# Kernel tuning notes

Measured on AMD Instinct MI355X. Metric: run time of the kernel, lower is better.

## Reference

```python
import jax, jax.numpy as jnp
import numpy as np

B, CIN, W = 4, 3, 28          # batch, in_channels, image size (= max_pos_embedding)
MID, HEADS, G, COUT = 16, 8, 4, 64
HALF = MID // 2               # row / col embedding dims


def _embed(u, w1, b1, gamma, beta, w2, b2):
    """Positional-embedding MLP applied elementwise to scalars u (N,).
    Conv2d(1->16,k=1) -> LayerNorm(16 channels) -> Swish -> Conv2d(16->MID/2,k=1)."""
    h = u[:, None] * w1[None, :] + b1                     # (N, 16)
    mu = h.mean(-1, keepdims=True)
    var = ((h - mu) ** 2).mean(-1, keepdims=True)
    h = gamma * (h - mu) / jnp.sqrt(var + 1e-5) + beta    # LayerNorm over channels
    h = h * jax.nn.sigmoid(h)                             # Swish
    return h @ w2.T + b2                                  # (N, HALF)


def _rot_indices():
    """Acted relative-position lookup indices for the 4 rotations.
    Values index into u = concat(rel, -rel) where rel = linspace(-1,1,2W-1)."""
    n = 2 * W - 1
    ar = np.arange(W)
    rel = ar[None, :] - ar[:, None] + (W - 1)             # rel[i,k] in [0, 2W-2]
    R = np.broadcast_to(rel[:, None, :, None], (W,) * 4)  # depends on (i,k)
    C = np.broadcast_to(rel[None, :, None, :], (W,) * 4)  # depends on (j,l)
    # rotation by 0/90/180/270 deg acting on (row, col) relative coordinates
    ridx = np.stack([R, C + n, R + n, C], 0)              # row component index
    cidx = np.stack([C, R, C + n, R + n], 0)              # col component index
    return jnp.asarray(ridx, jnp.int32), jnp.asarray(cidx, jnp.int32)


def setup_inputs() -> dict:
    key = jax.random.key(0)
    ks = jax.random.split(key, 24)
    def nrm(k, shape, fan):
        return jax.random.normal(k, shape, jnp.float32) / np.float32(np.sqrt(fan))
    inp = {"x": jax.random.normal(ks[0], (B, CIN, W, W), jnp.float32)}
    inp["wq"] = nrm(ks[1], (MID * HEADS, CIN), CIN); inp["bq"] = jnp.zeros((MID * HEADS,), jnp.float32)
    inp["wk"] = nrm(ks[2], (MID * HEADS, CIN), CIN); inp["bk"] = jnp.zeros((MID * HEADS,), jnp.float32)
    inp["wv"] = nrm(ks[3], (MID * HEADS, CIN), CIN); inp["bv"] = jnp.zeros((MID * HEADS,), jnp.float32)
    inp["w_out"] = nrm(ks[4], (COUT, MID * HEADS), MID * HEADS); inp["b_out"] = jnp.zeros((COUT,), jnp.float32)
    for pfx, base in (("row", 5), ("col", 12)):
        inp[f"{pfx}_w1"] = nrm(ks[base], (16,), 1)
        inp[f"{pfx}_b1"] = jnp.zeros((16,), jnp.float32)
        inp[f"{pfx}_gamma"] = jnp.ones((16,), jnp.float32)
        inp[f"{pfx}_beta"] = jnp.zeros((16,), jnp.float32)
        inp[f"{pfx}_w2"] = nrm(ks[base + 1], (HALF, 16), 16)
        inp[f"{pfx}_b2"] = jnp.zeros((HALF,), jnp.float32)
    inp["ridx"], inp["cidx"] = _rot_indices()
    return inp


def reference(x, wq, bq, wk, bk, wv, bv, w_out, b_out,
              row_w1, row_b1, row_gamma, row_beta, row_w2, row_b2,
              col_w1, col_b1, col_gamma, col_beta, col_w2, col_b2,
              ridx, cidx):
    b, c, H, Wd = x.shape
    # 1x1-conv q/k/v, viewed as (b, mid, heads, H, W)
    q = (jnp.einsum('oc,bcij->boij', wq, x) + bq[:, None, None]).reshape(b, MID, HEADS, H, Wd)
    k_ = (jnp.einsum('oc,bcij->boij', wk, x) + bk[:, None, None]).reshape(b, MID, HEADS, H, Wd)
    v = (jnp.einsum('oc,bcij->boij', wv, x) + bv[:, None, None]).reshape(b, MID, HEADS, H, Wd)

    content = jnp.einsum('bmhij,bmhkl->bhijkl', q, k_)     # (b,h,i,j,k,l)

    lin = jnp.linspace(-1.0, 1.0, 2 * Wd - 1)
    u = jnp.concatenate([lin, -lin])                       # unique relative coords
    E_row = _embed(u, row_w1, row_b1, row_gamma, row_beta, row_w2, row_b2)
    E_col = _embed(u, col_w1, col_b1, col_gamma, col_beta, col_w2, col_b2)
    row_emb = E_row[ridx]                                  # (G,i,j,k,l,HALF)
    col_emb = E_col[cidx]

    scores = jnp.einsum('bmhij,gijklm->bhgijkl', q[:, :HALF], row_emb)
    scores = scores + jnp.einsum('bmhij,gijklm->bhgijkl', q[:, HALF:], col_emb)
    scores = (scores + content[:, :, None]) / np.float32(np.sqrt(c))

    sh = scores.shape                                      # softmax over flattened (k,l)
    probs = jax.nn.softmax(scores.reshape(sh[:-2] + (-1,)), axis=-1).reshape(sh)

    out_v = jnp.einsum('bhgijkl,bmhkl->bmhgij', probs, v)  # (b,mid,heads,G,i,j)
    out_v = out_v.reshape(b, MID * HEADS, G, H, Wd)
    out = jnp.einsum('om,bmgij->bogij', w_out, out_v) + b_out[:, None, None, None]
    return out
```

## Files before the change

### kernel.cpp

```cpp
#include <hip/hip_runtime.h>
#include <hip/hip_fp16.h>

#define NPOS 784
#define WDIM 28

typedef _Float16 f16x8 __attribute__((ext_vector_type(8)));
typedef _Float16 f16x4 __attribute__((ext_vector_type(4)));
typedef float    f32x4 __attribute__((ext_vector_type(4)));

__global__ __launch_bounds__(256) void prep_kernel(
    const float* __restrict__ x,
    const float* __restrict__ wk, const float* __restrict__ bk,
    const float* __restrict__ wv, const float* __restrict__ bv,
    const float* __restrict__ w_out,
    const float* __restrict__ rw1, const float* __restrict__ rb1,
    const float* __restrict__ rga, const float* __restrict__ rbe,
    const float* __restrict__ rw2, const float* __restrict__ rb2,
    const float* __restrict__ cw1, const float* __restrict__ cb1,
    const float* __restrict__ cga, const float* __restrict__ cbe,
    const float* __restrict__ cw2, const float* __restrict__ cb2,
    _Float16* __restrict__ Kfrag, _Float16* __restrict__ Vfrag,
    _Float16* __restrict__ Wfrag,
    float* __restrict__ Etr, float* __restrict__ Etc)
{
    const int t = threadIdx.x;
    if (blockIdx.x == 416) {
        int d = -1;
        const float *w1 = rw1, *b1 = rb1, *ga = rga, *be = rbe, *w2 = rw2, *b2 = rb2;
        float* E = Etr;
        if (t < 110) { d = t; }
        else if (t >= 128 && t < 238) { d = t - 128; w1 = cw1; b1 = cb1; ga = cga; be = cbe; w2 = cw2; b2 = cb2; E = Etc; }
        if (d < 0) return;
        float u = (d < 55) ? (-1.0f + (float)d * (2.0f / 54.0f))
                           : -(-1.0f + (float)(d - 55) * (2.0f / 54.0f));
        float hb[16], mu = 0.0f;
#pragma unroll
        for (int c = 0; c < 16; ++c) { hb[c] = u * w1[c] + b1[c]; mu += hb[c]; }
        mu *= (1.0f / 16.0f);
        float var = 0.0f;
#pragma unroll
        for (int c = 0; c < 16; ++c) { float dv = hb[c] - mu; var += dv * dv; }
        var *= (1.0f / 16.0f);
        float rstd = rsqrtf(var + 1e-5f);
#pragma unroll
        for (int c = 0; c < 16; ++c) {
            float hn = ga[c] * (hb[c] - mu) * rstd + be[c];
            hb[c] = hn / (1.0f + __expf(-hn));
        }
#pragma unroll
        for (int m = 0; m < 8; ++m) {
            float e = b2[m];
#pragma unroll
            for (int c = 0; c < 16; ++c) e += hb[c] * w2[m * 16 + c];
            E[m * 110 + d] = e;
        }
        return;
    }
    if (blockIdx.x == 417) {
        for (int idx = t; idx < 8192; idx += 256) {
            int obc = idx >> 9, lane = (idx >> 3) & 63, j = idx & 7;
            int o  = (obc >> 2) * 16 + (lane & 15);
            int mh = (obc & 3) * 32 + (lane >> 4) * 8 + j;
            Wfrag[idx] = (_Float16)w_out[o * 128 + mh];
        }
        return;
    }

    const int bid  = blockIdx.x;
    const int b    = bid / 104, rem = bid - b * 104;
    const int tile = rem >> 3, h = rem & 7;
    const int lane = t & 63, mg = t >> 6;
    const int bh   = b * 8 + h;

    {
        if (t < 128) {
            int sub = (t >> 5) & 3, l32 = 32 + (t & 31);
            int qz = tile * 4 + sub;
            if (qz < 49)
                *(f16x8*)(Kfrag + ((size_t)(bh * 49 + qz) * 64 + l32) * 8) = (f16x8){};
        }
        if (tile == 12 && t < 32)
            *(f16x8*)(Vfrag + ((size_t)(bh * 25 + 24) * 64 + 32 + t) * 8) = (f16x8){};
    }

    const int ij = tile * 64 + lane;
    if (ij >= NPOS) return;

    float x0 = x[(b * 3 + 0) * NPOS + ij];
    float x1 = x[(b * 3 + 1) * NPOS + ij];
    float x2 = x[(b * 3 + 2) * NPOS + ij];

    float4 kv;
    float vv[4];
#pragma unroll
    for (int j = 0; j < 4; ++j) {
        int m = mg * 4 + j, oc = m * 8 + h;
        float w0, w1, w2v;
        w0 = wk[oc*3+0]; w1 = wk[oc*3+1]; w2v = wk[oc*3+2];
        ((float*)&kv)[j] = bk[oc] + w0*x0 + w1*x1 + w2v*x2;
        w0 = wv[oc*3+0]; w1 = wv[oc*3+1]; w2v = wv[oc*3+2];
        vv[j] = bv[oc] + w0*x0 + w1*x1 + w2v*x2;
    }
    {
        int qt = ij >> 4;
        int lp = ((mg >> 1) << 4) | (ij & 15);
        int jb = (mg & 1) * 4;
        f16x4 k4 = {(_Float16)kv.x, (_Float16)kv.y, (_Float16)kv.z, (_Float16)kv.w};
        *(f16x4*)(Kfrag + ((size_t)(bh * 49 + qt) * 64 + lp) * 8 + jb) = k4;
    }
    {
        int s5 = ij >> 5, kk = ij & 31;
        _Float16* vb = Vfrag + (((size_t)(bh * 25 + s5) * 64 + ((kk >> 3) << 4)) << 3) + (kk & 7);
#pragma unroll
        for (int j = 0; j < 4; ++j) vb[(mg * 4 + j) * 8] = (_Float16)vv[j];
    }
}

__global__ __launch_bounds__(512, 1) void attn_kernel(
    const _Float16* __restrict__ Kfrag, const _Float16* __restrict__ Vfrag,
    const _Float16* __restrict__ Wfrag,
    const float* __restrict__ Etr, const float* __restrict__ Etc,
    const float* __restrict__ x,
    const float* __restrict__ wq, const float* __restrict__ bq,
    const float* __restrict__ b_out, float* __restrict__ out)
{
    __shared__ __align__(16) unsigned char smem[56320 + 41472];
    const int t = threadIdx.x, wave = t >> 6, lane = t & 63;
    const int q15 = lane & 15, rg = lane >> 4;

    int bid = blockIdx.x;
    int xcd = bid & 7;
    int lb  = ((xcd < 4) ? xcd * 25 : 100 + (xcd - 4) * 24) + (bid >> 3);
    const int b = lb / 49, qt = lb - b * 49;
    const int bh = b * 8 + wave;
    const int q_ij = qt * 16 + q15;
    const int iq = q_ij / WDIM, jq = q_ij % WDIM;
    const float scale = 0.57735026918962576f;

    float* ebuf = (float*)(smem + 56320);
    for (int i = t; i < 1760; i += 512) ebuf[i] = (i < 880) ? Etr[i] : Etc[i - 880];

    float ql[8], qh[8];
    {
        float x0 = x[(b * 3 + 0) * NPOS + q_ij];
        float x1 = x[(b * 3 + 1) * NPOS + q_ij];
        float x2 = x[(b * 3 + 2) * NPOS + q_ij];
#pragma unroll
        for (int m = 0; m < 8; ++m) {
            int oc = m * 8 + wave;
            ql[m] = bq[oc] + wq[oc*3+0]*x0 + wq[oc*3+1]*x1 + wq[oc*3+2]*x2;
        }
#pragma unroll
        for (int m = 0; m < 8; ++m) {
            int oc = (m + 8) * 8 + wave;
            qh[m] = bq[oc] + wq[oc*3+0]*x0 + wq[oc*3+1]*x1 + wq[oc*3+2]*x2;
        }
    }
    f16x8 qf = {};
    if (rg == 0) {
#pragma unroll
        for (int j = 0; j < 8; ++j) qf[j] = (_Float16)ql[j];
    } else if (rg == 1) {
#pragma unroll
        for (int j = 0; j < 8; ++j) qf[j] = (_Float16)qh[j];
    }
    __syncthreads();

    {
        float mr = -3.0e38f, mc = -3.0e38f, m5r = -3.0e38f, m5c = -3.0e38f;
        for (int tv = 0; tv < 14; ++tv) {
            int dd = rg * 14 + tv;
            if (dd < 55) {
                float ar = 0, ac = 0, ar5 = 0, ac5 = 0;
#pragma unroll
                for (int mm = 0; mm < 8; ++mm) {
                    ar  += ql[mm] * ebuf[mm * 110 + dd];
                    ar5 += ql[mm] * ebuf[mm * 110 + dd + 55];
                    ac  += qh[mm] * ebuf[880 + mm * 110 + dd];
                    ac5 += qh[mm] * ebuf[880 + mm * 110 + dd + 55];
                }
                mr  = fmaxf(mr, ar);  mc  = fmaxf(mc, ac);
                m5r = fmaxf(m5r, ar5); m5c = fmaxf(m5c, ac5);
            }
        }
        mr  = fmaxf(mr,  __shfl_xor(mr, 16, 64));  mr  = fmaxf(mr,  __shfl_xor(mr, 32, 64));
        mc  = fmaxf(mc,  __shfl_xor(mc, 16, 64));  mc  = fmaxf(mc,  __shfl_xor(mc, 32, 64));
        m5r = fmaxf(m5r, __shfl_xor(m5r, 16, 64)); m5r = fmaxf(m5r, __shfl_xor(m5r, 32, 64));
        m5c = fmaxf(m5c, __shfl_xor(m5c, 16, 64)); m5c = fmaxf(m5c, __shfl_xor(m5c, 32, 64));
        uint2* tabw = (uint2*)smem + (wave * 16 + q15) * 55;
        for (int tv = 0; tv < 14; ++tv) {
            int dd = rg * 14 + tv;
            if (dd < 55) {
                float ar = 0, ac = 0, ar5 = 0, ac5 = 0;
#pragma unroll
                for (int mm = 0; mm < 8; ++mm) {
                    ar  += ql[mm] * ebuf[mm * 110 + dd];
                    ar5 += ql[mm] * ebuf[mm * 110 + dd + 55];
                    ac  += qh[mm] * ebuf[880 + mm * 110 + dd];
                    ac5 += qh[mm] * ebuf[880 + mm * 110 + dd + 55];
                }
                __half2 h01 = __floats2half2_rn(__expf(scale * (ar - mr)),
                                                __expf(scale * (ac - mc)));
                __half2 h23 = __floats2half2_rn(__expf(scale * (ar5 - m5r)),
                                                __expf(scale * (ac5 - m5c)));
                uint2 w; w.x = *(unsigned int*)&h01; w.y = *(unsigned int*)&h23;
                tabw[dd] = w;
            }
        }
    }
    __syncthreads();

    const f16x8* kchunk = (const f16x8*)(Kfrag + (size_t)bh * 49 * 64 * 8);

    float mx = -3.0e38f;
#pragma unroll 7
    for (int ch = 0; ch < 49; ++ch) {
        f16x8 kf = kchunk[ch * 64 + lane];
        f32x4 s = __builtin_amdgcn_mfma_f32_16x16x32_f16(kf, qf, (f32x4){0,0,0,0}, 0, 0, 0);
        mx = fmaxf(mx, fmaxf(fmaxf(s[0], s[1]), fmaxf(s[2], s[3])));
    }
    mx = fmaxf(mx, __shfl_xor(mx, 16, 64));
    mx = fmaxf(mx, __shfl_xor(mx, 32, 64));

    float ps0 = 0, ps1 = 0, ps2 = 0, ps3 = 0;
    f32x4 d0 = {0,0,0,0}, d1 = {0,0,0,0}, d2 = {0,0,0,0}, d3 = {0,0,0,0};
    _Float16* ptw = (_Float16*)(smem + 56320) + (size_t)wave * 2592;
    const uint2* tab = (const uint2*)smem + (wave * 16 + q15) * 55;
    const int prow  = (q15 & 3) * 4;
    const int tbase = (q15 >> 2) * 648;
    const f16x8* vbase = (const f16x8*)(Vfrag + (size_t)bh * 25 * 64 * 8);

    f16x8 kfA = kchunk[0 * 64 + lane];
    f16x8 kfB = kchunk[1 * 64 + lane];
    f16x8 bf  = vbase[lane];
    for (int pv = 0; pv < 25; ++pv) {
        int nA = (pv * 2 + 2 < 49) ? pv * 2 + 2 : 48;
        int nB = (pv * 2 + 3 < 49) ? pv * 2 + 3 : 48;
        int nV = (pv + 1 < 25) ? pv + 1 : 24;
        f16x8 kfA2 = kchunk[nA * 64 + lane];
        f16x8 kfB2 = kchunk[nB * 64 + lane];
        f16x8 bf2  = vbase[nV * 64 + lane];
#pragma unroll
        for (int c2 = 0; c2 < 2; ++c2) {
            int ch = pv * 2 + c2;
            float pg[4][4];
            if (ch < 49) {
                f16x8 kf = c2 ? kfB : kfA;
                f32x4 s = __builtin_amdgcn_mfma_f32_16x16x32_f16(kf, qf, (f32x4){0,0,0,0}, 0, 0, 0);
#pragma unroll
                for (int reg = 0; reg < 4; ++reg) {
                    float ec = __expf((s[reg] - mx) * scale) * 64.0f;
                    int k = ch * 16 + rg * 4 + reg;
                    int rk = (k * 2341) >> 16;
                    int ck = k - rk * WDIM;
                    uint2 tr = tab[rk - iq + 27];
                    uint2 tc = tab[ck - jq + 27];
                    float2 r01 = __half22float2(*(__half2*)&tr.x);
                    float2 r23 = __half22float2(*(__half2*)&tr.y);
                    float2 c01 = __half22float2(*(__half2*)&tc.x);
                    float2 c23 = __half22float2(*(__half2*)&tc.y);
                    pg[0][reg] = ec * r01.x * c01.y;
                    pg[1][reg] = ec * r01.y * c23.x;
                    pg[2][reg] = ec * r23.x * c23.y;
                    pg[3][reg] = ec * r23.y * c01.x;
                    ps0 += pg[0][reg]; ps1 += pg[1][reg];
                    ps2 += pg[2][reg]; ps3 += pg[3][reg];
                }
            } else {
#pragma unroll
                for (int g = 0; g < 4; ++g)
#pragma unroll
                    for (int reg = 0; reg < 4; ++reg) pg[g][reg] = 0.0f;
            }
            int cb = rg * 4 + c2 * 16;
#pragma unroll
            for (int g = 0; g < 4; ++g) {
                __half2 a01 = __floats2half2_rn(pg[g][0], pg[g][1]);
                __half2 a23 = __floats2half2_rn(pg[g][2], pg[g][3]);
                uint2 w; w.x = *(unsigned int*)&a01; w.y = *(unsigned int*)&a23;
                *(uint2*)(ptw + tbase + (prow + g) * 40 + cb) = w;
            }
        }
        f16x8 aA = *(const f16x8*)(ptw + 0 * 648 + q15 * 40 + rg * 8);
        d0 = __builtin_amdgcn_mfma_f32_16x16x32_f16(aA, bf, d0, 0, 0, 0);
        f16x8 aB = *(const f16x8*)(ptw + 1 * 648 + q15 * 40 + rg * 8);
        d1 = __builtin_amdgcn_mfma_f32_16x16x32_f16(aB, bf, d1, 0, 0, 0);
        f16x8 aC = *(const f16x8*)(ptw + 2 * 648 + q15 * 40 + rg * 8);
        d2 = __builtin_amdgcn_mfma_f32_16x16x32_f16(aC, bf, d2, 0, 0, 0);
        f16x8 aD = *(const f16x8*)(ptw + 3 * 648 + q15 * 40 + rg * 8);
        d3 = __builtin_amdgcn_mfma_f32_16x16x32_f16(aD, bf, d3, 0, 0, 0);
        kfA = kfA2; kfB = kfB2; bf = bf2;
    }
    ps0 += __shfl_xor(ps0, 16, 64); ps0 += __shfl_xor(ps0, 32, 64);
    ps1 += __shfl_xor(ps1, 16, 64); ps1 += __shfl_xor(ps1, 32, 64);
    ps2 += __shfl_xor(ps2, 16, 64); ps2 += __shfl_xor(ps2, 32, 64);
    ps3 += __shfl_xor(ps3, 16, 64); ps3 += __shfl_xor(ps3, 32, 64);
    float i0 = 1.0f / ps0, i1 = 1.0f / ps1, i2 = 1.0f / ps2, i3 = 1.0f / ps3;

    __syncthreads();
    _Float16* ovh = (_Float16*)(smem + 56320);
    {
        int mo = q15 * 8 + wave;
        int sq;
        sq = rg;
        ovh[(0*16 + sq)*136 + mo] = (_Float16)(d0[0] * __shfl(i0, sq, 64));
        ovh[(1*16 + sq)*136 + mo] = (_Float16)(d0[1] * __shfl(i1, sq, 64));
        ovh[(2*16 + sq)*136 + mo] = (_Float16)(d0[2] * __shfl(i2, sq, 64));
        ovh[(3*16 + sq)*136 + mo] = (_Float16)(d0[3] * __shfl(i3, sq, 64));
        sq = 4 + rg;
        ovh[(0*16 + sq)*136 + mo] = (_Float16)(d1[0] * __shfl(i0, sq, 64));
        ovh[(1*16 + sq)*136 + mo] = (_Float16)(d1[1] * __shfl(i1, sq, 64));
        ovh[(2*16 + sq)*136 + mo] = (_Float16)(d1[2] * __shfl(i2, sq, 64));
        ovh[(3*16 + sq)*136 + mo] = (_Float16)(d1[3] * __shfl(i3, sq, 64));
        sq = 8 + rg;
        ovh[(0*16 + sq)*136 + mo] = (_Float16)(d2[0] * __shfl(i0, sq, 64));
        ovh[(1*16 + sq)*136 + mo] = (_Float16)(d2[1] * __shfl(i1, sq, 64));
        ovh[(2*16 + sq)*136 + mo] = (_Float16)(d2[2] * __shfl(i2, sq, 64));
        ovh[(3*16 + sq)*136 + mo] = (_Float16)(d2[3] * __shfl(i3, sq, 64));
        sq = 12 + rg;
        ovh[(0*16 + sq)*136 + mo] = (_Float16)(d3[0] * __shfl(i0, sq, 64));
        ovh[(1*16 + sq)*136 + mo] = (_Float16)(d3[1] * __shfl(i1, sq, 64));
        ovh[(2*16 + sq)*136 + mo] = (_Float16)(d3[2] * __shfl(i3 == i3 ? i2 : i2, sq, 64) * 0.0f + d3[2] * __shfl(i2, sq, 64));
        ovh[(3*16 + sq)*136 + mo] = (_Float16)(d3[3] * __shfl(i3, sq, 64));
    }
    __syncthreads();

#pragma unroll
    for (int tt2 = 0; tt2 < 2; ++tt2) {
        int tl = wave * 2 + tt2;
        int ob = tl >> 2, g = tl & 3;
        f32x4 dd = {0,0,0,0};
#pragma unroll
        for (int c = 0; c < 4; ++c) {
            f16x8 wa = *(const f16x8*)(Wfrag + ((size_t)((ob * 4 + c) * 64 + lane)) * 8);
            f16x8 vb = *(const f16x8*)(ovh + (g * 16 + q15) * 136 + c * 32 + rg * 8);
            dd = __builtin_amdgcn_mfma_f32_16x16x32_f16(wa, vb, dd, 0, 0, 0);
        }
#pragma unroll
        for (int reg = 0; reg < 4; ++reg) {
            int o = ob * 16 + rg * 4 + reg;
            out[((size_t)(b * 64 + o) * 4 + g) * NPOS + qt * 16 + q15] = dd[reg] + b_out[o];
        }
    }
}

extern "C" void kernel_launch(void* const* d_in, const int* in_sizes, int n_in,
                              void* d_out, int out_size, void* d_ws, size_t ws_size,
                              hipStream_t stream)
{
    const float* x     = (const float*)d_in[0];
    const float* wq    = (const float*)d_in[1];
    const float* bq    = (const float*)d_in[2];
    const float* wk    = (const float*)d_in[3];
    const float* bk    = (const float*)d_in[4];
    const float* wv    = (const float*)d_in[5];
    const float* bv    = (const float*)d_in[6];
    const float* w_out = (const float*)d_in[7];
    const float* b_out = (const float*)d_in[8];
    const float* rw1 = (const float*)d_in[9];
    const float* rb1 = (const float*)d_in[10];
    const float* rga = (const float*)d_in[11];
    const float* rbe = (const float*)d_in[12];
    const float* rw2 = (const float*)d_in[13];
    const float* rb2 = (const float*)d_in[14];
    const float* cw1 = (const float*)d_in[15];
    const float* cb1 = (const float*)d_in[16];
    const float* cga = (const float*)d_in[17];
    const float* cbe = (const float*)d_in[18];
    const float* cw2 = (const float*)d_in[19];
    const float* cb2 = (const float*)d_in[20];

    float* Etr       = (float*)d_ws;
    float* Etc       = Etr + 880;
    _Float16* Kfrag  = (_Float16*)(Etc + 880);
    _Float16* Vfrag  = Kfrag + 802816;
    _Float16* Wfrag  = Vfrag + 409600;

    prep_kernel<<<418, 256, 0, stream>>>(x, wk, bk, wv, bv, w_out,
                                         rw1, rb1, rga, rbe, rw2, rb2,
                                         cw1, cb1, cga, cbe, cw2, cb2,
                                         Kfrag, Vfrag, Wfrag, Etr, Etc);
    attn_kernel<<<196, 512, 0, stream>>>(Kfrag, Vfrag, Wfrag, Etr, Etc,
                                         x, wq, bq, b_out, (float*)d_out);
}
```

Measured before the change: 158.8 us.

## Split key range across two wave groups per head with LDS reduction

```diff
diff --git a/kernel.cpp b/kernel.cpp
--- a/kernel.cpp
+++ b/kernel.cpp
@@ -116,7 +116,10 @@
     }
 }
 
-__global__ __launch_bounds__(512, 1) void attn_kernel(
+#define UNI_OFF 56320
+#define MX_OFF  97280
+#define PS_OFF  98304
+__global__ __launch_bounds__(1024, 1) void attn_kernel(
     const _Float16* __restrict__ Kfrag, const _Float16* __restrict__ Vfrag,
     const _Float16* __restrict__ Wfrag,
     const float* __restrict__ Etr, const float* __restrict__ Etc,
@@ -124,21 +127,22 @@
     const float* __restrict__ wq, const float* __restrict__ bq,
     const float* __restrict__ b_out, float* __restrict__ out)
 {
-    __shared__ __align__(16) unsigned char smem[56320 + 41472];
+    __shared__ __align__(16) unsigned char smem[100352];
     const int t = threadIdx.x, wave = t >> 6, lane = t & 63;
     const int q15 = lane & 15, rg = lane >> 4;
+    const int h = wave & 7, hf = wave >> 3;
 
     int bid = blockIdx.x;
     int xcd = bid & 7;
     int lb  = ((xcd < 4) ? xcd * 25 : 100 + (xcd - 4) * 24) + (bid >> 3);
     const int b = lb / 49, qt = lb - b * 49;
-    const int bh = b * 8 + wave;
+    const int bh = b * 8 + h;
     const int q_ij = qt * 16 + q15;
     const int iq = q_ij / WDIM, jq = q_ij % WDIM;
     const float scale = 0.57735026918962576f;
 
-    float* ebuf = (float*)(smem + 56320);
-    for (int i = t; i < 1760; i += 512) ebuf[i] = (i < 880) ? Etr[i] : Etc[i - 880];
+    float* ebuf = (float*)(smem + UNI_OFF);
+    for (int i = t; i < 1760; i += 1024) ebuf[i] = (i < 880) ? Etr[i] : Etc[i - 880];
 
     float ql[8], qh[8];
     {
@@ -147,12 +151,12 @@
         float x2 = x[(b * 3 + 2) * NPOS + q_ij];
 #pragma unroll
         for (int m = 0; m < 8; ++m) {
-            int oc = m * 8 + wave;
+            int oc = m * 8 + h;
             ql[m] = bq[oc] + wq[oc*3+0]*x0 + wq[oc*3+1]*x1 + wq[oc*3+2]*x2;
         }
 #pragma unroll
         for (int m = 0; m < 8; ++m) {
-            int oc = (m + 8) * 8 + wave;
+            int oc = (m + 8) * 8 + h;
             qh[m] = bq[oc] + wq[oc*3+0]*x0 + wq[oc*3+1]*x1 + wq[oc*3+2]*x2;
         }
     }
@@ -167,44 +171,35 @@
     __syncthreads();
 
     {
-        float mr = -3.0e38f, mc = -3.0e38f, m5r = -3.0e38f, m5c = -3.0e38f;
+        unsigned int* tab32 = (unsigned int*)smem + (h * 16 + q15) * 110;
+        const int d5 = hf * 55;
+        float m1 = -3.0e38f, m2 = -3.0e38f;
         for (int tv = 0; tv < 14; ++tv) {
             int dd = rg * 14 + tv;
             if (dd < 55) {
-                float ar = 0, ac = 0, ar5 = 0, ac5 = 0;
+                float a1 = 0, a2 = 0;
 #pragma unroll
                 for (int mm = 0; mm < 8; ++mm) {
-                    ar  += ql[mm] * ebuf[mm * 110 + dd];
-                    ar5 += ql[mm] * ebuf[mm * 110 + dd + 55];
-                    ac  += qh[mm] * ebuf[880 + mm * 110 + dd];
-                    ac5 += qh[mm] * ebuf[880 + mm * 110 + dd + 55];
+                    a1 += ql[mm] * ebuf[mm * 110 + dd + d5];
+                    a2 += qh[mm] * ebuf[880 + mm * 110 + dd + d5];
                 }
-                mr  = fmaxf(mr, ar);  mc  = fmaxf(mc, ac);
-                m5r = fmaxf(m5r, ar5); m5c = fmaxf(m5c, ac5);
+                m1 = fmaxf(m1, a1); m2 = fmaxf(m2, a2);
             }
         }
-        mr  = fmaxf(mr,  __shfl_xor(mr, 16, 64));  mr  = fmaxf(mr,  __shfl_xor(mr, 32, 64));
-        mc  = fmaxf(mc,  __shfl_xor(mc, 16, 64));  mc  = fmaxf(mc,  __shfl_xor(mc, 32, 64));
-        m5r = fmaxf(m5r, __shfl_xor(m5r, 16, 64)); m5r = fmaxf(m5r, __shfl_xor(m5r, 32, 64));
-        m5c = fmaxf(m5c, __shfl_xor(m5c, 16, 64)); m5c = fmaxf(m5c, __shfl_xor(m5c, 32, 64));
-        uint2* tabw = (uint2*)smem + (wave * 16 + q15) * 55;
+        m1 = fmaxf(m1, __shfl_xor(m1, 16, 64)); m1 = fmaxf(m1, __shfl_xor(m1, 32, 64));
+        m2 = fmaxf(m2, __shfl_xor(m2, 16, 64)); m2 = fmaxf(m2, __shfl_xor(m2, 32, 64));
         for (int tv = 0; tv < 14; ++tv) {
             int dd = rg * 14 + tv;
             if (dd < 55) {
-                float ar = 0, ac = 0, ar5 = 0, ac5 = 0;
+                float a1 = 0, a2 = 0;
 #pragma unroll
                 for (int mm = 0; mm < 8; ++mm) {
-                    ar  += ql[mm] * ebuf[mm * 110 + dd];
-                    ar5 += ql[mm] * ebuf[mm * 110 + dd + 55];
-                    ac  += qh[mm] * ebuf[880 + mm * 110 + dd];
-                    ac5 += qh[mm] * ebuf[880 + mm * 110 + dd + 55];
+                    a1 += ql[mm] * ebuf[mm * 110 + dd + d5];
+                    a2 += qh[mm] * ebuf[880 + mm * 110 + dd + d5];
                 }
-                __half2 h01 = __floats2half2_rn(__expf(scale * (ar - mr)),
-                                                __expf(scale * (ac - mc)));
-                __half2 h23 = __floats2half2_rn(__expf(scale * (ar5 - m5r)),
-                                                __expf(scale * (ac5 - m5c)));
-                uint2 w; w.x = *(unsigned int*)&h01; w.y = *(unsigned int*)&h23;
-                tabw[dd] = w;
+                __half2 hp = __floats2half2_rn(__expf(scale * (a1 - m1)),
+                                               __expf(scale * (a2 - m2)));
+                tab32[dd * 2 + hf] = *(unsigned int*)&hp;
             }
         }
     }
@@ -213,40 +208,52 @@
     const f16x8* kchunk = (const f16x8*)(Kfrag + (size_t)bh * 49 * 64 * 8);
 
     float mx = -3.0e38f;
-#pragma unroll 7
-    for (int ch = 0; ch < 49; ++ch) {
-        f16x8 kf = kchunk[ch * 64 + lane];
-        f32x4 s = __builtin_amdgcn_mfma_f32_16x16x32_f16(kf, qf, (f32x4){0,0,0,0}, 0, 0, 0);
-        mx = fmaxf(mx, fmaxf(fmaxf(s[0], s[1]), fmaxf(s[2], s[3])));
+#pragma unroll 5
+    for (int i = 0; i < 25; ++i) {
+        int ch = 2 * i + hf;
+        if (ch < 49) {
+            f16x8 kf = kchunk[ch * 64 + lane];
+            f32x4 s = __builtin_amdgcn_mfma_f32_16x16x32_f16(kf, qf, (f32x4){0,0,0,0}, 0, 0, 0);
+            mx = fmaxf(mx, fmaxf(fmaxf(s[0], s[1]), fmaxf(s[2], s[3])));
+        }
     }
     mx = fmaxf(mx, __shfl_xor(mx, 16, 64));
     mx = fmaxf(mx, __shfl_xor(mx, 32, 64));
+    float* mxbuf = (float*)(smem + MX_OFF);
+    if (rg == 0) mxbuf[wave * 16 + q15] = mx;
+    __syncthreads();
+    mx = fmaxf(mx, mxbuf[(wave ^ 8) * 16 + q15]);
 
     float ps0 = 0, ps1 = 0, ps2 = 0, ps3 = 0;
     f32x4 d0 = {0,0,0,0}, d1 = {0,0,0,0}, d2 = {0,0,0,0}, d3 = {0,0,0,0};
-    _Float16* ptw = (_Float16*)(smem + 56320) + (size_t)wave * 2592;
-    const uint2* tab = (const uint2*)smem + (wave * 16 + q15) * 55;
-    const int prow  = (q15 & 3) * 4;
-    const int tbase = (q15 >> 2) * 648;
+    _Float16* ptw = (_Float16*)(smem + UNI_OFF) + wave * 1280;
+    const uint2* tab = (const uint2*)smem + (h * 16 + q15) * 55;
     const f16x8* vbase = (const f16x8*)(Vfrag + (size_t)bh * 25 * 64 * 8);
-
-    f16x8 kfA = kchunk[0 * 64 + lane];
-    f16x8 kfB = kchunk[1 * 64 + lane];
-    f16x8 bf  = vbase[lane];
-    for (int pv = 0; pv < 25; ++pv) {
-        int nA = (pv * 2 + 2 < 49) ? pv * 2 + 2 : 48;
-        int nB = (pv * 2 + 3 < 49) ? pv * 2 + 3 : 48;
-        int nV = (pv + 1 < 25) ? pv + 1 : 24;
+    const int wco = q15 * 40 + rg * 4;
+    const int rco = (lane & 15) * 40 + (lane >> 4) * 8;
+
+    int pv = hf;
+    f16x8 kfA = kchunk[(2 * pv) * 64 + lane];
+    f16x8 kfB = kchunk[(2 * pv + 1) * 64 + lane];
+    f16x8 bf  = vbase[pv * 64 + lane];
+    for (int i = 0; i < 13; ++i) {
+        int pvn = pv + 2;
+        int nA = (pvn * 2     < 49) ? pvn * 2     : 48;
+        int nB = (pvn * 2 + 1 < 49) ? pvn * 2 + 1 : 48;
+        int nV = (pvn < 25) ? pvn : 24;
         f16x8 kfA2 = kchunk[nA * 64 + lane];
         f16x8 kfB2 = kchunk[nB * 64 + lane];
         f16x8 bf2  = vbase[nV * 64 + lane];
+
+        uint2 pk0[4], pk1[4];
 #pragma unroll
         for (int c2 = 0; c2 < 2; ++c2) {
             int ch = pv * 2 + c2;
-            float pg[4][4];
+            uint2* pk = c2 ? pk1 : pk0;
             if (ch < 49) {
                 f16x8 kf = c2 ? kfB : kfA;
                 f32x4 s = __builtin_amdgcn_mfma_f32_16x16x32_f16(kf, qf, (f32x4){0,0,0,0}, 0, 0, 0);
+                float pg[4][4];
 #pragma unroll
                 for (int reg = 0; reg < 4; ++reg) {
                     float ec = __expf((s[reg] - mx) * scale) * 64.0f;
@@ -266,69 +273,80 @@
                     ps0 += pg[0][reg]; ps1 += pg[1][reg];
                     ps2 += pg[2][reg]; ps3 += pg[3][reg];
                 }
+#pragma unroll
+                for (int g = 0; g < 4; ++g) {
+                    __half2 a01 = __floats2half2_rn(pg[g][0], pg[g][1]);
+                    __half2 a23 = __floats2half2_rn(pg[g][2], pg[g][3]);
+                    pk[g].x = *(unsigned int*)&a01; pk[g].y = *(unsigned int*)&a23;
+                }
             } else {
 #pragma unroll
-                for (int g = 0; g < 4; ++g)
-#pragma unroll
-                    for (int reg = 0; reg < 4; ++reg) pg[g][reg] = 0.0f;
+                for (int g = 0; g < 4; ++g) { pk[g].x = 0u; pk[g].y = 0u; }
             }
-            int cb = rg * 4 + c2 * 16;
-#pragma unroll
-            for (int g = 0; g < 4; ++g) {
-                __half2 a01 = __floats2half2_rn(pg[g][0], pg[g][1]);
-                __half2 a23 = __floats2half2_rn(pg[g][2], pg[g][3]);
-                uint2 w; w.x = *(unsigned int*)&a01; w.y = *(unsigned int*)&a23;
-                *(uint2*)(ptw + tbase + (prow + g) * 40 + cb) = w;
-            }
-        }
-        f16x8 aA = *(const f16x8*)(ptw + 0 * 648 + q15 * 40 + rg * 8);
-        d0 = __builtin_amdgcn_mfma_f32_16x16x32_f16(aA, bf, d0, 0, 0, 0);
-        f16x8 aB = *(const f16x8*)(ptw + 1 * 648 + q15 * 40 + rg * 8);
-        d1 = __builtin_amdgcn_mfma_f32_16x16x32_f16(aB, bf, d1, 0, 0, 0);
-        f16x8 aC = *(const f16x8*)(ptw + 2 * 648 + q15 * 40 + rg * 8);
-        d2 = __builtin_amdgcn_mfma_f32_16x16x32_f16(aC, bf, d2, 0, 0, 0);
-        f16x8 aD = *(const f16x8*)(ptw + 3 * 648 + q15 * 40 + rg * 8);
-        d3 = __builtin_amdgcn_mfma_f32_16x16x32_f16(aD, bf, d3, 0, 0, 0);
-        kfA = kfA2; kfB = kfB2; bf = bf2;
+        }
+        _Float16* b0 = ptw;
+        _Float16* b1 = ptw + 640;
+        *(uint2*)(b0 + wco) = pk0[0]; *(uint2*)(b0 + wco + 16) = pk1[0];
+        *(uint2*)(b1 + wco) = pk0[1]; *(uint2*)(b1 + wco + 16) = pk1[1];
+        { f16x8 a = *(const f16x8*)(b0 + rco);
+          d0 = __builtin_amdgcn_mfma_f32_16x16x32_f16(a, bf, d0, 0, 0, 0); }
+        *(uint2*)(b0 + wco) = pk0[2]; *(uint2*)(b0 + wco + 16) = pk1[2];
+        { f16x8 a = *(const f16x8*)(b1 + rco);
+          d1 = __builtin_amdgcn_mfma_f32_16x16x32_f16(a, bf, d1, 0, 0, 0); }
+        *(uint2*)(b1 + wco) = pk0[3]; *(uint2*)(b1 + wco + 16) = pk1[3];
+        { f16x8 a = *(const f16x8*)(b0 + rco);
+          d2 = __builtin_amdgcn_mfma_f32_16x16x32_f16(a, bf, d2, 0, 0, 0); }
+        { f16x8 a = *(const f16x8*)(b1 + rco);
+          d3 = __builtin_amdgcn_mfma_f32_16x16x32_f16(a, bf, d3, 0, 0, 0); }
+        kfA = kfA2; kfB = kfB2; bf = bf2; pv = pvn;
     }
     ps0 += __shfl_xor(ps0, 16, 64); ps0 += __shfl_xor(ps0, 32, 64);
     ps1 += __shfl_xor(ps1, 16, 64); ps1 += __shfl_xor(ps1, 32, 64);
     ps2 += __shfl_xor(ps2, 16, 64); ps2 += __shfl_xor(ps2, 32, 64);
     ps3 += __shfl_xor(ps3, 16, 64); ps3 += __shfl_xor(ps3, 32, 64);
-    float i0 = 1.0f / ps0, i1 = 1.0f / ps1, i2 = 1.0f / ps2, i3 = 1.0f / ps3;
-
-    __syncthreads();
-    _Float16* ovh = (_Float16*)(smem + 56320);
-    {
-        int mo = q15 * 8 + wave;
-        int sq;
-        sq = rg;
-        ovh[(0*16 + sq)*136 + mo] = (_Float16)(d0[0] * __shfl(i0, sq, 64));
-        ovh[(1*16 + sq)*136 + mo] = (_Float16)(d0[1] * __shfl(i1, sq, 64));
-        ovh[(2*16 + sq)*136 + mo] = (_Float16)(d0[2] * __shfl(i2, sq, 64));
-        ovh[(3*16 + sq)*136 + mo] = (_Float16)(d0[3] * __shfl(i3, sq, 64));
-        sq = 4 + rg;
-        ovh[(0*16 + sq)*136 + mo] = (_Float16)(d1[0] * __shfl(i0, sq, 64));
-        ovh[(1*16 + sq)*136 + mo] = (_Float16)(d1[1] * __shfl(i1, sq, 64));
-        ovh[(2*16 + sq)*136 + mo] = (_Float16)(d1[2] * __shfl(i2, sq, 64));
-        ovh[(3*16 + sq)*136 + mo] = (_Float16)(d1[3] * __shfl(i3, sq, 64));
-        sq = 8 + rg;
-        ovh[(0*16 + sq)*136 + mo] = (_Float16)(d2[0] * __shfl(i0, sq, 64));
-        ovh[(1*16 + sq)*136 + mo] = (_Float16)(d2[1] * __shfl(i1, sq, 64));
-        ovh[(2*16 + sq)*136 + mo] = (_Float16)(d2[2] * __shfl(i2, sq, 64));
-        ovh[(3*16 + sq)*136 + mo] = (_Float16)(d2[3] * __shfl(i3, sq, 64));
-        sq = 12 + rg;
-        ovh[(0*16 + sq)*136 + mo] = (_Float16)(d3[0] * __shfl(i0, sq, 64));
-        ovh[(1*16 + sq)*136 + mo] = (_Float16)(d3[1] * __shfl(i1, sq, 64));
-        ovh[(2*16 + sq)*136 + mo] = (_Float16)(d3[2] * __shfl(i3 == i3 ? i2 : i2, sq, 64) * 0.0f + d3[2] * __shfl(i2, sq, 64));
-        ovh[(3*16 + sq)*136 + mo] = (_Float16)(d3[3] * __shfl(i3, sq, 64));
-    }
-    __syncthreads();
-
-#pragma unroll
-    for (int tt2 = 0; tt2 < 2; ++tt2) {
-        int tl = wave * 2 + tt2;
-        int ob = tl >> 2, g = tl & 3;
+
+    __syncthreads();
+    float* dbuf = (float*)(smem + UNI_OFF);
+    float* psb  = (float*)(smem + PS_OFF);
+    if (hf) {
+        float* ds = dbuf + (wave - 8) * (64 * 17) + lane * 17;
+        ds[0]=d0[0];  ds[1]=d0[1];  ds[2]=d0[2];  ds[3]=d0[3];
+        ds[4]=d1[0];  ds[5]=d1[1];  ds[6]=d1[2];  ds[7]=d1[3];
+        ds[8]=d2[0];  ds[9]=d2[1];  ds[10]=d2[2]; ds[11]=d2[3];
+        ds[12]=d3[0]; ds[13]=d3[1]; ds[14]=d3[2]; ds[15]=d3[3];
+        if (rg == 0) {
+            float* pp = psb + (wave - 8) * 64 + q15 * 4;
+            pp[0] = ps0; pp[1] = ps1; pp[2] = ps2; pp[3] = ps3;
+        }
+    }
+    __syncthreads();
+    if (!hf) {
+        const float* ds = dbuf + wave * (64 * 17) + lane * 17;
+        d0[0]+=ds[0];  d0[1]+=ds[1];  d0[2]+=ds[2];  d0[3]+=ds[3];
+        d1[0]+=ds[4];  d1[1]+=ds[5];  d1[2]+=ds[6];  d1[3]+=ds[7];
+        d2[0]+=ds[8];  d2[1]+=ds[9];  d2[2]+=ds[10]; d2[3]+=ds[11];
+        d3[0]+=ds[12]; d3[1]+=ds[13]; d3[2]+=ds[14]; d3[3]+=ds[15];
+        const float* pp = psb + wave * 64 + q15 * 4;
+        ps0 += pp[0]; ps1 += pp[1]; ps2 += pp[2]; ps3 += pp[3];
+    }
+    __syncthreads();
+    _Float16* ovh = (_Float16*)(smem + UNI_OFF);
+    if (!hf) {
+        float i0 = 1.0f / ps0, i1 = 1.0f / ps1, i2 = 1.0f / ps2, i3 = 1.0f / ps3;
+        int mo = q15 * 8 + h;
+#pragma unroll
+        for (int reg = 0; reg < 4; ++reg) {
+            int q = rg * 4 + reg;
+            ovh[(0*16 + q)*136 + mo] = (_Float16)(d0[reg] * __shfl(i0, q, 64));
+            ovh[(1*16 + q)*136 + mo] = (_Float16)(d1[reg] * __shfl(i1, q, 64));
+            ovh[(2*16 + q)*136 + mo] = (_Float16)(d2[reg] * __shfl(i2, q, 64));
+            ovh[(3*16 + q)*136 + mo] = (_Float16)(d3[reg] * __shfl(i3, q, 64));
+        }
+    }
+    __syncthreads();
+
+    {
+        int ob = wave >> 2, g = wave & 3;
         f32x4 dd = {0,0,0,0};
 #pragma unroll
         for (int c = 0; c < 4; ++c) {
@@ -380,6 +398,6 @@
                                          rw1, rb1, rga, rbe, rw2, rb2,
                                          cw1, cb1, cga, cbe, cw2, cb2,
                                          Kfrag, Vfrag, Wfrag, Etr, Etc);
-    attn_kernel<<<196, 512, 0, stream>>>(Kfrag, Vfrag, Wfrag, Etr, Etc,
-                                         x, wq, bq, b_out, (float*)d_out);
+    attn_kernel<<<196, 1024, 0, stream>>>(Kfrag, Vfrag, Wfrag, Etr, Etc,
+                                          x, wq, bq, b_out, (float*)d_out);
 }
```

New measurement: 161.4 us. Within noise of the previous version (+1.6%).

## Double-buffer probability tiles and compute softmax denominators via MFMA with ones

Applied to the files above, without the earlier changes.

```diff
diff --git a/kernel.cpp b/kernel.cpp
--- a/kernel.cpp
+++ b/kernel.cpp
@@ -116,6 +116,7 @@
     }
 }
 
+#define UNI_OFF 56320
 __global__ __launch_bounds__(512, 1) void attn_kernel(
     const _Float16* __restrict__ Kfrag, const _Float16* __restrict__ Vfrag,
     const _Float16* __restrict__ Wfrag,
@@ -124,7 +125,7 @@
     const float* __restrict__ wq, const float* __restrict__ bq,
     const float* __restrict__ b_out, float* __restrict__ out)
 {
-    __shared__ __align__(16) unsigned char smem[56320 + 41472];
+    __shared__ __align__(16) unsigned char smem[56320 + 82944];
     const int t = threadIdx.x, wave = t >> 6, lane = t & 63;
     const int q15 = lane & 15, rg = lane >> 4;
 
@@ -137,7 +138,7 @@
     const int iq = q_ij / WDIM, jq = q_ij % WDIM;
     const float scale = 0.57735026918962576f;
 
-    float* ebuf = (float*)(smem + 56320);
+    float* ebuf = (float*)(smem + UNI_OFF);
     for (int i = t; i < 1760; i += 512) ebuf[i] = (i < 880) ? Etr[i] : Etc[i - 880];
 
     float ql[8], qh[8];
@@ -221,19 +222,32 @@
     }
     mx = fmaxf(mx, __shfl_xor(mx, 16, 64));
     mx = fmaxf(mx, __shfl_xor(mx, 32, 64));
-
-    float ps0 = 0, ps1 = 0, ps2 = 0, ps3 = 0;
+    const float c1  = 0.57735026918962576f * 1.44269504088896341f;
+    const float c2f = 6.0f - mx * c1;
+
     f32x4 d0 = {0,0,0,0}, d1 = {0,0,0,0}, d2 = {0,0,0,0}, d3 = {0,0,0,0};
-    _Float16* ptw = (_Float16*)(smem + 56320) + (size_t)wave * 2592;
+    f32x4 e0 = {0,0,0,0}, e1 = {0,0,0,0}, e2 = {0,0,0,0}, e3 = {0,0,0,0};
+    _Float16* ptw = (_Float16*)(smem + UNI_OFF) + (size_t)wave * 5184;
     const uint2* tab = (const uint2*)smem + (wave * 16 + q15) * 55;
     const int prow  = (q15 & 3) * 4;
     const int tbase = (q15 >> 2) * 648;
+    const int rof   = q15 * 40 + rg * 8;
     const f16x8* vbase = (const f16x8*)(Vfrag + (size_t)bh * 25 * 64 * 8);
+    f16x8 onesB;
+#pragma unroll
+    for (int j = 0; j < 8; ++j) onesB[j] = (_Float16)1.0f;
 
     f16x8 kfA = kchunk[0 * 64 + lane];
     f16x8 kfB = kchunk[1 * 64 + lane];
-    f16x8 bf  = vbase[lane];
+    f16x8 bfCur = vbase[lane];
+    f16x8 bfPrev = {};
     for (int pv = 0; pv < 25; ++pv) {
+        _Float16*       wbuf = ptw + (pv & 1) * 2592;
+        const _Float16* rbuf = ptw + ((pv & 1) ^ 1) * 2592;
+        f16x8 aA = *(const f16x8*)(rbuf + 0 * 648 + rof);
+        f16x8 aB = *(const f16x8*)(rbuf + 1 * 648 + rof);
+        f16x8 aC = *(const f16x8*)(rbuf + 2 * 648 + rof);
+        f16x8 aD = *(const f16x8*)(rbuf + 3 * 648 + rof);
         int nA = (pv * 2 + 2 < 49) ? pv * 2 + 2 : 48;
         int nB = (pv * 2 + 3 < 49) ? pv * 2 + 3 : 48;
         int nV = (pv + 1 < 25) ? pv + 1 : 24;
@@ -243,13 +257,14 @@
 #pragma unroll
         for (int c2 = 0; c2 < 2; ++c2) {
             int ch = pv * 2 + c2;
-            float pg[4][4];
+            int cb = rg * 4 + c2 * 16;
             if (ch < 49) {
                 f16x8 kf = c2 ? kfB : kfA;
                 f32x4 s = __builtin_amdgcn_mfma_f32_16x16x32_f16(kf, qf, (f32x4){0,0,0,0}, 0, 0, 0);
+                float pg[4][4];
 #pragma unroll
                 for (int reg = 0; reg < 4; ++reg) {
-                    float ec = __expf((s[reg] - mx) * scale) * 64.0f;
+                    float ec = exp2f(s[reg] * c1 + c2f);
                     int k = ch * 16 + rg * 4 + reg;
                     int rk = (k * 2341) >> 16;
                     int ck = k - rk * WDIM;
@@ -263,65 +278,68 @@
                     pg[1][reg] = ec * r01.y * c23.x;
                     pg[2][reg] = ec * r23.x * c23.y;
                     pg[3][reg] = ec * r23.y * c01.x;
-                    ps0 += pg[0][reg]; ps1 += pg[1][reg];
-                    ps2 += pg[2][reg]; ps3 += pg[3][reg];
+                }
+#pragma unroll
+                for (int g = 0; g < 4; ++g) {
+                    __half2 a01 = __floats2half2_rn(pg[g][0], pg[g][1]);
+                    __half2 a23 = __floats2half2_rn(pg[g][2], pg[g][3]);
+                    uint2 w; w.x = *(unsigned int*)&a01; w.y = *(unsigned int*)&a23;
+                    *(uint2*)(wbuf + tbase + (prow + g) * 40 + cb) = w;
                 }
             } else {
+                uint2 w; w.x = 0u; w.y = 0u;
 #pragma unroll
                 for (int g = 0; g < 4; ++g)
-#pragma unroll
-                    for (int reg = 0; reg < 4; ++reg) pg[g][reg] = 0.0f;
+                    *(uint2*)(wbuf + tbase + (prow + g) * 40 + cb) = w;
             }
-            int cb = rg * 4 + c2 * 16;
-#pragma unroll
-            for (int g = 0; g < 4; ++g) {
-                __half2 a01 = __floats2half2_rn(pg[g][0], pg[g][1]);
-                __half2 a23 = __floats2half2_rn(pg[g][2], pg[g][3]);
-                uint2 w; w.x = *(unsigned int*)&a01; w.y = *(unsigned int*)&a23;
-                *(uint2*)(ptw + tbase + (prow + g) * 40 + cb) = w;
-            }
-        }
-        f16x8 aA = *(const f16x8*)(ptw + 0 * 648 + q15 * 40 + rg * 8);
-        d0 = __builtin_amdgcn_mfma_f32_16x16x32_f16(aA, bf, d0, 0, 0, 0);
-        f16x8 aB = *(const f16x8*)(ptw + 1 * 648 + q15 * 40 + rg * 8);
-        d1 = __builtin_amdgcn_mfma_f32_16x16x32_f16(aB, bf, d1, 0, 0, 0);
-        f16x8 aC = *(const f16x8*)(ptw + 2 * 648 + q15 * 40 + rg * 8);
-        d2 = __builtin_amdgcn_mfma_f32_16x16x32_f16(aC, bf, d2, 0, 0, 0);
-        f16x8 aD = *(const f16x8*)(ptw + 3 * 648 + q15 * 40 + rg * 8);
-        d3 = __builtin_amdgcn_mfma_f32_16x16x32_f16(aD, bf, d3, 0, 0, 0);
-        kfA = kfA2; kfB = kfB2; bf = bf2;
-    }
-    ps0 += __shfl_xor(ps0, 16, 64); ps0 += __shfl_xor(ps0, 32, 64);
-    ps1 += __shfl_xor(ps1, 16, 64); ps1 += __shfl_xor(ps1, 32, 64);
-    ps2 += __shfl_xor(ps2, 16, 64); ps2 += __shfl_xor(ps2, 32, 64);
-    ps3 += __shfl_xor(ps3, 16, 64); ps3 += __shfl_xor(ps3, 32, 64);
-    float i0 = 1.0f / ps0, i1 = 1.0f / ps1, i2 = 1.0f / ps2, i3 = 1.0f / ps3;
+        }
+        if (pv) {
+            __builtin_amdgcn_s_setprio(1);
+            d0 = __builtin_amdgcn_mfma_f32_16x16x32_f16(aA, bfPrev, d0, 0, 0, 0);
+            e0 = __builtin_amdgcn_mfma_f32_16x16x32_f16(aA, onesB,  e0, 0, 0, 0);
+            d1 = __builtin_amdgcn_mfma_f32_16x16x32_f16(aB, bfPrev, d1, 0, 0, 0);
+            e1 = __builtin_amdgcn_mfma_f32_16x16x32_f16(aB, onesB,  e1, 0, 0, 0);
+            d2 = __builtin_amdgcn_mfma_f32_16x16x32_f16(aC, bfPrev, d2, 0, 0, 0);
+            e2 = __builtin_amdgcn_mfma_f32_16x16x32_f16(aC, onesB,  e2, 0, 0, 0);
+            d3 = __builtin_amdgcn_mfma_f32_16x16x32_f16(aD, bfPrev, d3, 0, 0, 0);
+            e3 = __builtin_amdgcn_mfma_f32_16x16x32_f16(aD, onesB,  e3, 0, 0, 0);
+            __builtin_amdgcn_s_setprio(0);
+        }
+        kfA = kfA2; kfB = kfB2; bfPrev = bfCur; bfCur = bf2;
+    }
+    {
+        const _Float16* rbuf = ptw;
+        f16x8 aA = *(const f16x8*)(rbuf + 0 * 648 + rof);
+        f16x8 aB = *(const f16x8*)(rbuf + 1 * 648 + rof);
+        f16x8 aC = *(const f16x8*)(rbuf + 2 * 648 + rof);
+        f16x8 aD = *(const f16x8*)(rbuf + 3 * 648 + rof);
+        __builtin_amdgcn_s_setprio(1);
+        d0 = __builtin_amdgcn_mfma_f32_16x16x32_f16(aA, bfPrev, d0, 0, 0, 0);
+        e0 = __builtin_amdgcn_mfma_f32_16x16x32_f16(aA, onesB,  e0, 0, 0, 0);
+        d1 = __builtin_amdgcn_mfma_f32_16x16x32_f16(aB, bfPrev, d1, 0, 0, 0);
+        e1 = __builtin_amdgcn_mfma_f32_16x16x32_f16(aB, onesB,  e1, 0, 0, 0);
+        d2 = __builtin_amdgcn_mfma_f32_16x16x32_f16(aC, bfPrev, d2, 0, 0, 0);
+        e2 = __builtin_amdgcn_mfma_f32_16x16x32_f16(aC, onesB,  e2, 0, 0, 0);
+        d3 = __builtin_amdgcn_mfma_f32_16x16x32_f16(aD, bfPrev, d3, 0, 0, 0);
+        e3 = __builtin_amdgcn_mfma_f32_16x16x32_f16(aD, onesB,  e3, 0, 0, 0);
+        __builtin_amdgcn_s_setprio(0);
+    }
 
     __syncthreads();
-    _Float16* ovh = (_Float16*)(smem + 56320);
+    _Float16* ovh = (_Float16*)(smem + UNI_OFF);
     {
         int mo = q15 * 8 + wave;
-        int sq;
-        sq = rg;
-        ovh[(0*16 + sq)*136 + mo] = (_Float16)(d0[0] * __shfl(i0, sq, 64));
-        ovh[(1*16 + sq)*136 + mo] = (_Float16)(d0[1] * __shfl(i1, sq, 64));
-        ovh[(2*16 + sq)*136 + mo] = (_Float16)(d0[2] * __shfl(i2, sq, 64));
-        ovh[(3*16 + sq)*136 + mo] = (_Float16)(d0[3] * __shfl(i3, sq, 64));
-        sq = 4 + rg;
-        ovh[(0*16 + sq)*136 + mo] = (_Float16)(d1[0] * __shfl(i0, sq, 64));
-        ovh[(1*16 + sq)*136 + mo] = (_Float16)(d1[1] * __shfl(i1, sq, 64));
-        ovh[(2*16 + sq)*136 + mo] = (_Float16)(d1[2] * __shfl(i2, sq, 64));
-        ovh[(3*16 + sq)*136 + mo] = (_Float16)(d1[3] * __shfl(i3, sq, 64));
-        sq = 8 + rg;
-        ovh[(0*16 + sq)*136 + mo] = (_Float16)(d2[0] * __shfl(i0, sq, 64));
-        ovh[(1*16 + sq)*136 + mo] = (_Float16)(d2[1] * __shfl(i1, sq, 64));
-        ovh[(2*16 + sq)*136 + mo] = (_Float16)(d2[2] * __shfl(i2, sq, 64));
-        ovh[(3*16 + sq)*136 + mo] = (_Float16)(d2[3] * __shfl(i3, sq, 64));
-        sq = 12 + rg;
-        ovh[(0*16 + sq)*136 + mo] = (_Float16)(d3[0] * __shfl(i0, sq, 64));
-        ovh[(1*16 + sq)*136 + mo] = (_Float16)(d3[1] * __shfl(i1, sq, 64));
-        ovh[(2*16 + sq)*136 + mo] = (_Float16)(d3[2] * __shfl(i3 == i3 ? i2 : i2, sq, 64) * 0.0f + d3[2] * __shfl(i2, sq, 64));
-        ovh[(3*16 + sq)*136 + mo] = (_Float16)(d3[3] * __shfl(i3, sq, 64));
+#pragma unroll
+        for (int reg = 0; reg < 4; ++reg) {
+            float i0 = (e0[reg] > 0.0f) ? 1.0f / e0[reg] : 0.0f;
+            float i1 = (e1[reg] > 0.0f) ? 1.0f / e1[reg] : 0.0f;
+            float i2 = (e2[reg] > 0.0f) ? 1.0f / e2[reg] : 0.0f;
+            float i3 = (e3[reg] > 0.0f) ? 1.0f / e3[reg] : 0.0f;
+            ovh[(reg * 16 +      rg) * 136 + mo] = (_Float16)(d0[reg] * i0);
+            ovh[(reg * 16 +  4 + rg) * 136 + mo] = (_Float16)(d1[reg] * i1);
+            ovh[(reg * 16 +  8 + rg) * 136 + mo] = (_Float16)(d2[reg] * i2);
+            ovh[(reg * 16 + 12 + rg) * 136 + mo] = (_Float16)(d3[reg] * i3);
+        }
     }
     __syncthreads();
 
```

Measured after the change: 156.2 us. No clear change (-1.6%).
